# Kernel tuning notes

Measured on AMD Instinct MI355X. Metric: run time of the kernel, lower is better.

The kernel has to match this reference:

```python
import jax, jax.numpy as jnp
import numpy as np

N_BITS = 8
QMAX = 2 ** (N_BITS - 1) - 1  # 127 for int8 symmetric


def fake_quant(x):
    """Per-token (last-dim) dynamic symmetric fake quantization (quant->dequant)."""
    scale = jnp.max(jnp.abs(x), axis=-1, keepdims=True) / QMAX
    scale = jnp.maximum(scale, 1e-8)
    q = jnp.clip(jnp.round(x / scale), -QMAX - 1, QMAX)
    return q * scale


def setup_inputs() -> dict:
    key = jax.random.key(0)
    k1, k2, k3, k4, k5 = jax.random.split(key, 5)
    B, T, D, H = 32, 1024, 1152, 4608
    x = jax.random.normal(k1, (B, T, D), dtype=jnp.float32)
    reorder_index = jnp.arange(D, dtype=jnp.int32)  # channel reorder permutation
    W1 = jax.random.normal(k2, (H, D), dtype=jnp.float32) * (1.0 / np.sqrt(D))
    b1 = jax.random.normal(k3, (H,), dtype=jnp.float32) * 0.02
    W2 = jax.random.normal(k4, (D, H), dtype=jnp.float32) * (1.0 / np.sqrt(H))
    b2 = jax.random.normal(k5, (D,), dtype=jnp.float32) * 0.02
    return {"x": x, "reorder_index": reorder_index, "W1": W1, "b1": b1, "W2": W2, "b2": b2}


def reference(x, reorder_index, W1, b1, W2, b2):
    # channel reorder (index_select on dim 2)
    x = jnp.take(x, reorder_index, axis=2)
    # input fake-quant
    x = fake_quant(x)
    # fc1 (torch Linear: x @ W.T + b)
    h = jnp.einsum("btd,hd->bth", x, W1) + b1
    # GELU activation (timm Mlp default); drop1/norm are Identity in eval
    h = jax.nn.gelu(h, approximate=False)
    # activation fake-quant
    h = fake_quant(h)
    # fc2
    out = jnp.einsum("bth,dh->btd", h, W2) + b2
    return out
```

## Files before the change

kernel.cpp:

```cpp
#include <hip/hip_runtime.h>
#include <cstdint>
#include <cstddef>


typedef __attribute__((ext_vector_type(8))) short short8;
typedef __attribute__((ext_vector_type(4))) float f32x4;

__device__ __forceinline__ float bf2f(unsigned short u) {
    return __uint_as_float(((unsigned)u) << 16);
}
__device__ __forceinline__ unsigned short f2bf(float f) {
    unsigned u = __float_as_uint(f);
    u += 0x7fff + ((u >> 16) & 1);
    return (unsigned short)(u >> 16);
}

__device__ __forceinline__ void gload_lds16(const void* gptr, void* ldsptr) {
    typedef __attribute__((address_space(1))) const unsigned int gu32;
    typedef __attribute__((address_space(3))) unsigned int lu32;
    __builtin_amdgcn_global_load_lds((gu32*)gptr, (lu32*)ldsptr, 16, 0, 0);
}

template <int BN, bool GELU>
__global__ __launch_bounds__(512, 2) void gemm8p(
    const unsigned short* __restrict__ A, const unsigned short* __restrict__ B,
    const float* __restrict__ bias, const float* __restrict__ rowScale,
    void* __restrict__ C, int M, int N, int K)
{
    constexpr int BM  = 256;
    constexpr int NR  = BN / 64;
    constexpr int WCN = BN / 4;
    constexpr int LB  = (BN * 32 * 2) / (512 * 16);

    __shared__ unsigned short lA[2][2][BM * 32];
    __shared__ unsigned short lB[2][2][BN * 32];

    const int tid  = threadIdx.x;
    const int lane = tid & 63;
    const int wave = tid >> 6;
    const int wm = wave >> 2;
    const int wn = wave & 3;
    const int wbase = wave << 6;

    const int nbn = N / BN;
    {
    }
    const int nwg = (int)gridDim.x;
    const int orig = (int)blockIdx.x;
    const int qs = nwg >> 3, rs = nwg & 7;
    const int xcd = orig & 7, loc = orig >> 3;
    const int wg = (xcd < rs ? xcd * (qs + 1) : rs * (qs + 1) + (xcd - rs) * qs) + loc;
    const int bn = wg % nbn;
    const int bm = wg / nbn;

    const unsigned short* Ab = A + (size_t)bm * BM * K;
    const unsigned short* Bb = B + (size_t)bn * BN * K;

    int srcA0, srcA1;
    {
        int idx = tid;       int r = idx >> 2, s = idx & 3;
        srcA0 = r * K + ((s ^ ((r >> 1) & 3)) << 3);
        idx = 512 + tid;     r = idx >> 2; s = idx & 3;
        srcA1 = r * K + ((s ^ ((r >> 1) & 3)) << 3);
    }

    auto stageA = [&](unsigned short* slab, int t, int kh) {
        const int ko = t * 64 + kh * 32;
        gload_lds16(Ab + srcA0 + ko, &slab[wbase * 8]);
        gload_lds16(Ab + srcA1 + ko, &slab[(512 + wbase) * 8]);
    };
    auto stageB = [&](unsigned short* slab, int t, int kh) {
        const int ko = t * 64 + kh * 32;
        gload_lds16(Bb + srcA0 + ko, &slab[wbase * 8]);
        if (LB == 2) gload_lds16(Bb + srcA1 + ko, &slab[(512 + wbase) * 8]);
    };

    const int q  = lane >> 4;
    const int lr = lane & 15;
    const int cidx = q ^ ((lr >> 1) & 3);
    const int laneOff = lr * 32 + cidx * 8;

    f32x4 acc[8][NR];
#pragma unroll
    for (int i = 0; i < 8; ++i)
#pragma unroll
        for (int j = 0; j < NR; ++j) acc[i][j] = (f32x4){0.f, 0.f, 0.f, 0.f};

    short8 bfrag[NR];

#define VM_WAIT()                                                            \
    do { if (BN == 256) asm volatile("s_waitcnt vmcnt(6)" ::: "memory");     \
         else           asm volatile("s_waitcnt vmcnt(4)" ::: "memory"); } while (0)

#define PH(RD, RKH, MH, STG_A, SD, SKH, STGT, VM_END)                                  \
    {                                                                                  \
        short8 af[4];                                                                  \
        if (MH == 0) {                                                                 \
            _Pragma("unroll")                                                          \
            for (int jj = 0; jj < NR; ++jj)                                            \
                bfrag[jj] = *(const short8*)&lB[RD][RKH][(wn * WCN + jj * 16) * 32 + laneOff]; \
        }                                                                              \
        _Pragma("unroll")                                                              \
        for (int ii = 0; ii < 4; ++ii)                                                 \
            af[ii] = *(const short8*)&lA[RD][RKH][(wm * 128 + MH * 64 + ii * 16) * 32 + laneOff]; \
        if (STG_A) stageA(&lA[SD][SKH][0], STGT, SKH);                                 \
        else       stageB(&lB[SD][SKH][0], STGT, SKH);                                 \
        asm volatile("" ::: "memory");                                                 \
        __builtin_amdgcn_s_barrier();                                                  \
        asm volatile("s_waitcnt lgkmcnt(0)" ::: "memory");                             \
        __builtin_amdgcn_s_setprio(1);                                                 \
        _Pragma("unroll")                                                              \
        for (int ii = 0; ii < 4; ++ii)                                                 \
            _Pragma("unroll")                                                          \
            for (int jj = 0; jj < NR; ++jj)                                            \
                acc[MH * 4 + ii][jj] = __builtin_amdgcn_mfma_f32_16x16x32_bf16(        \
                    af[ii], bfrag[jj], acc[MH * 4 + ii][jj], 0, 0, 0);                 \
        __builtin_amdgcn_s_setprio(0);                                                 \
        if (VM_END) VM_WAIT();                                                         \
        asm volatile("" ::: "memory");                                                 \
        __builtin_amdgcn_s_barrier();                                                  \
    }

    const int nt = K >> 6;
    const int nIter = nt >> 1;

    stageB(&lB[0][0][0], 0, 0);
    stageA(&lA[0][0][0], 0, 0);
    stageB(&lB[0][1][0], 0, 1);
    stageA(&lA[0][1][0], 0, 1);
    stageB(&lB[1][0][0], 1, 0);
    stageA(&lA[1][0][0], 1, 0);
    stageB(&lB[1][1][0], 1, 1);
    VM_WAIT();
    asm volatile("" ::: "memory");
    __builtin_amdgcn_s_barrier();

    for (int it = 0; it < nIter; ++it) {
        const int T  = it << 1;
        const int t2 = (T + 2 < nt) ? T + 2 : nt - 1;
        const int t3 = (T + 3 < nt) ? T + 3 : nt - 1;
        PH(0, 0, 0, true , 1, 1, T + 1, false)
        PH(0, 0, 1, false, 0, 0, t2,    false)
        PH(0, 1, 0, true , 0, 0, t2,    false)
        PH(0, 1, 1, false, 0, 1, t2,    true )
        PH(1, 0, 0, true , 0, 1, t2,    false)
        PH(1, 0, 1, false, 1, 0, t3,    false)
        PH(1, 1, 0, true , 1, 0, t3,    false)
        PH(1, 1, 1, false, 1, 1, t3,    true )
    }
#undef PH
#undef VM_WAIT

#pragma unroll
    for (int mi = 0; mi < 8; ++mi) {
#pragma unroll
        for (int r = 0; r < 4; ++r) {
            int m = bm * BM + wm * 128 + mi * 16 + q * 4 + r;
            float sc = rowScale[m];
#pragma unroll
            for (int j = 0; j < NR; ++j) {
                int n = bn * BN + wn * WCN + j * 16 + lr;
                float v = acc[mi][j][r] * sc + bias[n];
                size_t off = (size_t)m * N + n;
                if (GELU) {
                    v = 0.5f * v * (1.f + erff(v * 0.70710678118654752f));
                    ((unsigned short*)C)[off] = f2bf(v);
                } else {
                    ((float*)C)[off] = v;
                }
            }
        }
    }
}

__device__ __forceinline__ float waveMax(float m) {
#pragma unroll
    for (int off = 32; off; off >>= 1) m = fmaxf(m, __shfl_xor(m, off));
    return m;
}

__global__ __launch_bounds__(256) void quant_x_kernel(
    const float* __restrict__ x, const int* __restrict__ ridx,
    unsigned short* __restrict__ xq, float* __restrict__ sx, int D)
{
    __shared__ float buf[1152];
    __shared__ float wmax[4];
    const float* xr = x + (size_t)blockIdx.x * D;
    const int tid = threadIdx.x;
    float m = 0.f;
    for (int c = tid; c < D; c += 256) {
        float v = xr[ridx[c]];
        buf[c] = v;
        m = fmaxf(m, fabsf(v));
    }
    m = waveMax(m);
    if ((tid & 63) == 0) wmax[tid >> 6] = m;
    __syncthreads();
    m = fmaxf(fmaxf(wmax[0], wmax[1]), fmaxf(wmax[2], wmax[3]));
    float scale = fmaxf(m * (1.f / 127.f), 1e-8f);
    float inv = 1.f / scale;
    unsigned short* xo = xq + (size_t)blockIdx.x * D;
    for (int c = tid; c < D; c += 256) {
        float qv = fminf(fmaxf(rintf(buf[c] * inv), -128.f), 127.f);
        xo[c] = f2bf(qv);
    }
    if (tid == 0) sx[blockIdx.x] = scale;
}

__global__ __launch_bounds__(256) void quant_h_kernel(
    unsigned short* __restrict__ h, float* __restrict__ sh, int H)
{
    __shared__ float buf[4608];
    __shared__ float wmax[4];
    unsigned int* hr = (unsigned int*)(h + (size_t)blockIdx.x * H);
    const int tid = threadIdx.x;
    const int n2 = H >> 1;
    float m = 0.f;
    for (int c = tid; c < n2; c += 256) {
        unsigned int u = hr[c];
        float v0 = bf2f((unsigned short)(u & 0xffffu));
        float v1 = bf2f((unsigned short)(u >> 16));
        buf[2 * c] = v0; buf[2 * c + 1] = v1;
        m = fmaxf(m, fmaxf(fabsf(v0), fabsf(v1)));
    }
    m = waveMax(m);
    if ((tid & 63) == 0) wmax[tid >> 6] = m;
    __syncthreads();
    m = fmaxf(fmaxf(wmax[0], wmax[1]), fmaxf(wmax[2], wmax[3]));
    float scale = fmaxf(m * (1.f / 127.f), 1e-8f);
    float inv = 1.f / scale;
    for (int c = tid; c < n2; c += 256) {
        float q0 = fminf(fmaxf(rintf(buf[2 * c] * inv), -128.f), 127.f);
        float q1 = fminf(fmaxf(rintf(buf[2 * c + 1] * inv), -128.f), 127.f);
        hr[c] = (unsigned int)f2bf(q0) | ((unsigned int)f2bf(q1) << 16);
    }
    if (tid == 0) sh[blockIdx.x] = scale;
}

__global__ __launch_bounds__(256) void cvt_f32_bf16(
    const float* __restrict__ src, unsigned short* __restrict__ dst, long long n)
{
    long long i = ((long long)blockIdx.x * 256 + threadIdx.x) * 4;
    long long stride = (long long)gridDim.x * 1024;
    for (; i < n; i += stride) {
        float4 v = *(const float4*)(src + i);
        ushort4 o;
        o.x = f2bf(v.x); o.y = f2bf(v.y); o.z = f2bf(v.z); o.w = f2bf(v.w);
        *(ushort4*)(dst + i) = o;
    }
}

extern "C" void kernel_launch(void* const* d_in, const int* in_sizes, int n_in,
                              void* d_out, int out_size, void* d_ws, size_t ws_size,
                              hipStream_t stream)
{
    const float* x    = (const float*)d_in[0];
    const int*   ridx = (const int*)d_in[1];
    const float* W1   = (const float*)d_in[2];
    const float* b1   = (const float*)d_in[3];
    const float* W2   = (const float*)d_in[4];
    const float* b2   = (const float*)d_in[5];
    float* out = (float*)d_out;

    const long long D = in_sizes[1];
    const long long H = in_sizes[3];
    const long long M = (long long)in_sizes[0] / D;

    auto al = [](size_t v) { return (v + 255) & ~(size_t)255; };
    char* p = (char*)d_ws;
    unsigned short* w1b = (unsigned short*)p; p += al((size_t)(H * D * 2));
    unsigned short* w2b = (unsigned short*)p; p += al((size_t)(D * H * 2));
    size_t used = (size_t)(p - (char*)d_ws);

    size_t perTok = (size_t)(D + H) * 2 + 8;
    long long chunk = (long long)((ws_size - used - 4096) / perTok);
    chunk = (chunk / 256) * 256;
    if (chunk > M) chunk = M;
    if (chunk < 256) chunk = 256;

    unsigned short* xq   = (unsigned short*)p; p += al((size_t)chunk * D * 2);
    unsigned short* hbuf = (unsigned short*)p; p += al((size_t)chunk * H * 2);
    float* sx = (float*)p; p += al((size_t)chunk * 4);
    float* sh = (float*)p;

    cvt_f32_bf16<<<dim3((unsigned)((H * D) / 1024)), 256, 0, stream>>>(W1, w1b, H * D);
    cvt_f32_bf16<<<dim3((unsigned)((D * H) / 1024)), 256, 0, stream>>>(W2, w2b, D * H);

    for (long long r0 = 0; r0 < M; r0 += chunk) {
        long long mc = M - r0; if (mc > chunk) mc = chunk;
        quant_x_kernel<<<dim3((unsigned)mc), 256, 0, stream>>>(
            x + r0 * D, ridx, xq, sx, (int)D);
        unsigned nwg1 = (unsigned)((H / 256) * (mc / 256));
        gemm8p<256, true><<<dim3(nwg1), 512, 0, stream>>>(
            xq, w1b, b1, sx, hbuf, (int)mc, (int)H, (int)D);
        quant_h_kernel<<<dim3((unsigned)mc), 256, 0, stream>>>(hbuf, sh, (int)H);
        unsigned nwg2 = (unsigned)((D / 128) * (mc / 256));
        gemm8p<128, false><<<dim3(nwg2), 512, 0, stream>>>(
            hbuf, w2b, b2, sh, out + r0 * D, (int)mc, (int)D, (int)H);
    }
}
```

Measured before the change: 1.503 ms.

## Double-buffer LDS fragment registers to overlap reads with MFMA

Restructures the GEMM main loop so that each phase issues the LDS reads for the next phase's A/B fragments into alternate register sets while running MFMAs on fragments loaded in the previous phase. This drops one barrier and the lgkmcnt(0) wait per phase, and adjusts the vmcnt wait points and their counts. It also adds a prologue preload. It aims to hide LDS read latency behind matrix math, at the cost of more VGPRs, which may pressure occupancy under launch_bounds(512,2). It also relies on subtle barrier and wait-count correctness for LDS reuse, which risks races.

```diff
diff --git a/kernel.cpp b/kernel.cpp
--- a/kernel.cpp
+++ b/kernel.cpp
@@ -43,8 +43,6 @@
     const int wbase = wave << 6;
 
     const int nbn = N / BN;
-    {
-    }
     const int nwg = (int)gridDim.x;
     const int orig = (int)blockIdx.x;
     const int qs = nwg >> 3, rs = nwg & 7;
@@ -86,37 +84,37 @@
 #pragma unroll
         for (int j = 0; j < NR; ++j) acc[i][j] = (f32x4){0.f, 0.f, 0.f, 0.f};
 
-    short8 bfrag[NR];
-
-#define VM_WAIT()                                                            \
+    short8 afs0[4], afs1[4], bfs0[NR], bfs1[NR];
+
+#define VM_LOOP()                                                            \
+    do { if (BN == 256) asm volatile("s_waitcnt vmcnt(4)" ::: "memory");     \
+         else           asm volatile("s_waitcnt vmcnt(3)" ::: "memory"); } while (0)
+#define VM_PRO()                                                             \
     do { if (BN == 256) asm volatile("s_waitcnt vmcnt(6)" ::: "memory");     \
          else           asm volatile("s_waitcnt vmcnt(4)" ::: "memory"); } while (0)
 
-#define PH(RD, RKH, MH, STG_A, SD, SKH, STGT, VM_END)                                  \
+#define PH(MD, MKH, MMH, MAF, MBF, RDD, RKH, RMH, RAF, RBF, LOADB, STG_A, SD, SKH, STGT, VM) \
     {                                                                                  \
-        short8 af[4];                                                                  \
-        if (MH == 0) {                                                                 \
+        if (STG_A) stageA(&lA[SD][SKH][0], STGT, SKH);                                 \
+        else       stageB(&lB[SD][SKH][0], STGT, SKH);                                 \
+        if (LOADB) {                                                                   \
             _Pragma("unroll")                                                          \
             for (int jj = 0; jj < NR; ++jj)                                            \
-                bfrag[jj] = *(const short8*)&lB[RD][RKH][(wn * WCN + jj * 16) * 32 + laneOff]; \
+                RBF[jj] = *(const short8*)&lB[RDD][RKH][(wn * WCN + jj * 16) * 32 + laneOff]; \
         }                                                                              \
         _Pragma("unroll")                                                              \
         for (int ii = 0; ii < 4; ++ii)                                                 \
-            af[ii] = *(const short8*)&lA[RD][RKH][(wm * 128 + MH * 64 + ii * 16) * 32 + laneOff]; \
-        if (STG_A) stageA(&lA[SD][SKH][0], STGT, SKH);                                 \
-        else       stageB(&lB[SD][SKH][0], STGT, SKH);                                 \
-        asm volatile("" ::: "memory");                                                 \
-        __builtin_amdgcn_s_barrier();                                                  \
-        asm volatile("s_waitcnt lgkmcnt(0)" ::: "memory");                             \
+            RAF[ii] = *(const short8*)&lA[RDD][RKH][(wm * 128 + RMH * 64 + ii * 16) * 32 + laneOff]; \
+        __builtin_amdgcn_sched_barrier(0);                                             \
         __builtin_amdgcn_s_setprio(1);                                                 \
         _Pragma("unroll")                                                              \
         for (int ii = 0; ii < 4; ++ii)                                                 \
             _Pragma("unroll")                                                          \
             for (int jj = 0; jj < NR; ++jj)                                            \
-                acc[MH * 4 + ii][jj] = __builtin_amdgcn_mfma_f32_16x16x32_bf16(        \
-                    af[ii], bfrag[jj], acc[MH * 4 + ii][jj], 0, 0, 0);                 \
+                acc[MMH * 4 + ii][jj] = __builtin_amdgcn_mfma_f32_16x16x32_bf16(       \
+                    MAF[ii], MBF[jj], acc[MMH * 4 + ii][jj], 0, 0, 0);                 \
         __builtin_amdgcn_s_setprio(0);                                                 \
-        if (VM_END) VM_WAIT();                                                         \
+        if (VM) VM_LOOP();                                                             \
         asm volatile("" ::: "memory");                                                 \
         __builtin_amdgcn_s_barrier();                                                  \
     }
@@ -131,25 +129,32 @@
     stageB(&lB[1][0][0], 1, 0);
     stageA(&lA[1][0][0], 1, 0);
     stageB(&lB[1][1][0], 1, 1);
-    VM_WAIT();
+    VM_PRO();
     asm volatile("" ::: "memory");
     __builtin_amdgcn_s_barrier();
+#pragma unroll
+    for (int jj = 0; jj < NR; ++jj)
+        bfs0[jj] = *(const short8*)&lB[0][0][(wn * WCN + jj * 16) * 32 + laneOff];
+#pragma unroll
+    for (int ii = 0; ii < 4; ++ii)
+        afs1[ii] = *(const short8*)&lA[0][0][(wm * 128 + ii * 16) * 32 + laneOff];
 
     for (int it = 0; it < nIter; ++it) {
         const int T  = it << 1;
         const int t2 = (T + 2 < nt) ? T + 2 : nt - 1;
         const int t3 = (T + 3 < nt) ? T + 3 : nt - 1;
-        PH(0, 0, 0, true , 1, 1, T + 1, false)
-        PH(0, 0, 1, false, 0, 0, t2,    false)
-        PH(0, 1, 0, true , 0, 0, t2,    false)
-        PH(0, 1, 1, false, 0, 1, t2,    true )
-        PH(1, 0, 0, true , 0, 1, t2,    false)
-        PH(1, 0, 1, false, 1, 0, t3,    false)
-        PH(1, 1, 0, true , 1, 0, t3,    false)
-        PH(1, 1, 1, false, 1, 1, t3,    true )
+        PH(0,0,0, afs1,bfs0,  0,0,1, afs0,bfs1, false,  true , 1,1, T+1, false)
+        PH(0,0,1, afs0,bfs0,  0,1,0, afs1,bfs1, true ,  false, 0,0, t2,  false)
+        PH(0,1,0, afs1,bfs1,  0,1,1, afs0,bfs0, false,  true , 0,0, t2,  true )
+        PH(0,1,1, afs0,bfs1,  1,0,0, afs1,bfs0, true ,  false, 0,1, t2,  false)
+        PH(1,0,0, afs1,bfs0,  1,0,1, afs0,bfs1, false,  true , 0,1, t2,  false)
+        PH(1,0,1, afs0,bfs0,  1,1,0, afs1,bfs1, true ,  false, 1,0, t3,  false)
+        PH(1,1,0, afs1,bfs1,  1,1,1, afs0,bfs0, false,  true , 1,0, t3,  true )
+        PH(1,1,1, afs0,bfs1,  0,0,0, afs1,bfs0, true ,  false, 1,1, t3,  false)
     }
 #undef PH
-#undef VM_WAIT
+#undef VM_LOOP
+#undef VM_PRO
 
 #pragma unroll
     for (int mi = 0; mi < 8; ++mi) {
```

Measured after the change: 1.528 ms. No clear change (+1.7%).
